# Kernel optimization log

Hardware: AMD Instinct MI355X
Metric: run time of the kernel (lower is better)

## Reference

```python
import jax, jax.numpy as jnp
import numpy as np

LOG_2PI_PLUS_1 = float(np.log(2.0 * np.pi) + 1.0)


def setup_inputs() -> dict:
    key = jax.random.key(0)
    disanchor = jax.random.uniform(key, (4096, 8192), dtype=jnp.float32)
    return {"disanchor": disanchor}


def reference(disanchor) -> jnp.ndarray:
    m, n = disanchor.shape
    # masked log-sum over nonzero entries; guard log(0) to avoid nan
    nonzero = disanchor != 0
    safe = jnp.where(nonzero, disanchor, 1.0)
    sumD = jnp.sum(jnp.where(nonzero, jnp.log(safe), 0.0))
    total = (m * n / 2) * LOG_2PI_PLUS_1 + 0.5 * sumD
    # if total > 0: log(1 + total) else 1.0
    return jnp.where(total > 0, jnp.log1p(jnp.maximum(total, 0.0)), 1.0)
```

## Files before the change

kernel.cpp:

```cpp
#include <hip/hip_runtime.h>
#include <math.h>

#define LOG_2PI_PLUS_1 2.8378770664093454835606594728112

__global__ __launch_bounds__(256) void masked_logsum_kernel(
    const float* __restrict__ x, long long n, double* __restrict__ ws) {
  const long long n4 = n >> 2;
  const float4* __restrict__ x4 = (const float4*)x;
  long long tid = (long long)blockIdx.x * blockDim.x + threadIdx.x;
  long long stride = (long long)gridDim.x * blockDim.x;

  double acc = 0.0;
  for (long long i = tid; i < n4; i += stride) {
    float4 v = x4[i];
    float s = 0.0f;
    s += (v.x != 0.0f) ? __logf(v.x) : 0.0f;
    s += (v.y != 0.0f) ? __logf(v.y) : 0.0f;
    s += (v.z != 0.0f) ? __logf(v.z) : 0.0f;
    s += (v.w != 0.0f) ? __logf(v.w) : 0.0f;
    acc += (double)s;
  }

  if (tid == 0) {
    for (long long i = n4 << 2; i < n; ++i) {
      float v = x[i];
      acc += (double)((v != 0.0f) ? __logf(v) : 0.0f);
    }
  }

  #pragma unroll
  for (int off = 32; off > 0; off >>= 1) {
    acc += __shfl_down(acc, off, 64);
  }

  __shared__ double smem[4];
  const int lane = threadIdx.x & 63;
  const int wave = threadIdx.x >> 6;
  if (lane == 0) smem[wave] = acc;
  __syncthreads();
  if (threadIdx.x == 0) {
    double t = smem[0] + smem[1] + smem[2] + smem[3];
    atomicAdd(ws, t);
  }
}

__global__ void finalize_kernel(const double* __restrict__ ws,
                                float* __restrict__ out, double mn_half) {
  double total = mn_half * LOG_2PI_PLUS_1 + 0.5 * ws[0];
  out[0] = (total > 0.0) ? (float)log1p(total) : 1.0f;
}

extern "C" void kernel_launch(void* const* d_in, const int* in_sizes, int n_in,
                              void* d_out, int out_size, void* d_ws, size_t ws_size,
                              hipStream_t stream) {
  const float* x = (const float*)d_in[0];
  long long n = (long long)in_sizes[0];
  double* ws = (double*)d_ws;

  hipMemsetAsync(d_ws, 0, sizeof(double), stream);

  const int block = 256;
  const int grid = 2048;
  masked_logsum_kernel<<<grid, block, 0, stream>>>(x, n, ws);
  finalize_kernel<<<1, 1, 0, stream>>>(ws, (float*)d_out, 0.5 * (double)n);
}
```

Baseline: 200.9 us.

## Fuse finalize into reduction via last-block ticket and unroll loads by two

Removes the separate finalize kernel launch: each block increments an atomic ticket after adding its partial sum, and the last block computes the final log1p result. The main loop is also unrolled to issue two float4 loads per iteration with separate accumulators, giving more memory-level parallelism. Adds an extra atomic and thread fences per block, and assumes the workspace is large enough to hold the ticket counter.

```diff
diff --git a/kernel.cpp b/kernel.cpp
--- a/kernel.cpp
+++ b/kernel.cpp
@@ -3,27 +3,45 @@
 
 #define LOG_2PI_PLUS_1 2.8378770664093454835606594728112
 
-__global__ __launch_bounds__(256) void masked_logsum_kernel(
-    const float* __restrict__ x, long long n, double* __restrict__ ws) {
+__global__ __launch_bounds__(256) void fused_masked_logsum_kernel(
+    const float* __restrict__ x, long long n, double* __restrict__ ws,
+    float* __restrict__ out, double mn_half) {
   const long long n4 = n >> 2;
   const float4* __restrict__ x4 = (const float4*)x;
-  long long tid = (long long)blockIdx.x * blockDim.x + threadIdx.x;
-  long long stride = (long long)gridDim.x * blockDim.x;
+  const long long tid = (long long)blockIdx.x * blockDim.x + threadIdx.x;
+  const long long stride = (long long)gridDim.x * blockDim.x;
 
-  double acc = 0.0;
-  for (long long i = tid; i < n4; i += stride) {
-    float4 v = x4[i];
-    float s = 0.0f;
-    s += (v.x != 0.0f) ? __logf(v.x) : 0.0f;
-    s += (v.y != 0.0f) ? __logf(v.y) : 0.0f;
-    s += (v.z != 0.0f) ? __logf(v.z) : 0.0f;
-    s += (v.w != 0.0f) ? __logf(v.w) : 0.0f;
-    acc += (double)s;
+  double acc0 = 0.0, acc1 = 0.0;
+  long long i = tid;
+  for (; i + stride < n4; i += 2 * stride) {
+    float4 a = x4[i];
+    float4 b = x4[i + stride];
+    float sa = 0.0f, sb = 0.0f;
+    sa += (a.x != 0.0f) ? __logf(a.x) : 0.0f;
+    sa += (a.y != 0.0f) ? __logf(a.y) : 0.0f;
+    sa += (a.z != 0.0f) ? __logf(a.z) : 0.0f;
+    sa += (a.w != 0.0f) ? __logf(a.w) : 0.0f;
+    sb += (b.x != 0.0f) ? __logf(b.x) : 0.0f;
+    sb += (b.y != 0.0f) ? __logf(b.y) : 0.0f;
+    sb += (b.z != 0.0f) ? __logf(b.z) : 0.0f;
+    sb += (b.w != 0.0f) ? __logf(b.w) : 0.0f;
+    acc0 += (double)sa;
+    acc1 += (double)sb;
   }
+  for (; i < n4; i += stride) {
+    float4 a = x4[i];
+    float sa = 0.0f;
+    sa += (a.x != 0.0f) ? __logf(a.x) : 0.0f;
+    sa += (a.y != 0.0f) ? __logf(a.y) : 0.0f;
+    sa += (a.z != 0.0f) ? __logf(a.z) : 0.0f;
+    sa += (a.w != 0.0f) ? __logf(a.w) : 0.0f;
+    acc0 += (double)sa;
+  }
+  double acc = acc0 + acc1;
 
   if (tid == 0) {
-    for (long long i = n4 << 2; i < n; ++i) {
-      float v = x[i];
+    for (long long j = n4 << 2; j < n; ++j) {
+      float v = x[j];
       acc += (double)((v != 0.0f) ? __logf(v) : 0.0f);
     }
   }
@@ -38,16 +56,22 @@
   const int wave = threadIdx.x >> 6;
   if (lane == 0) smem[wave] = acc;
   __syncthreads();
+
   if (threadIdx.x == 0) {
     double t = smem[0] + smem[1] + smem[2] + smem[3];
     atomicAdd(ws, t);
+    __threadfence();
+    unsigned int* ticket = (unsigned int*)(ws + 1);
+    unsigned int prev = atomicAdd(ticket, 1u);
+    if (prev == gridDim.x - 1) {
+      __threadfence();
+      double sumD;
+      sumD = __longlong_as_double(
+          atomicAdd((unsigned long long*)ws, 0ull));
+      double total = mn_half * LOG_2PI_PLUS_1 + 0.5 * sumD;
+      out[0] = (total > 0.0) ? (float)log1p(total) : 1.0f;
+    }
   }
-}
-
-__global__ void finalize_kernel(const double* __restrict__ ws,
-                                float* __restrict__ out, double mn_half) {
-  double total = mn_half * LOG_2PI_PLUS_1 + 0.5 * ws[0];
-  out[0] = (total > 0.0) ? (float)log1p(total) : 1.0f;
 }
 
 extern "C" void kernel_launch(void* const* d_in, const int* in_sizes, int n_in,
@@ -57,10 +81,10 @@
   long long n = (long long)in_sizes[0];
   double* ws = (double*)d_ws;
 
-  hipMemsetAsync(d_ws, 0, sizeof(double), stream);
+  hipMemsetAsync(d_ws, 0, 16, stream);
 
   const int block = 256;
   const int grid = 2048;
-  masked_logsum_kernel<<<grid, block, 0, stream>>>(x, n, ws);
-  finalize_kernel<<<1, 1, 0, stream>>>(ws, (float*)d_out, 0.5 * (double)n);
+  fused_masked_logsum_kernel<<<grid, block, 0, stream>>>(
+      x, n, ws, (float*)d_out, 0.5 * (double)n);
 }
```

After: 269.4 us. 1.34x slower.
